# Kernel optimization log

Hardware: AMD Instinct MI355X
Metric: run time of the kernel (lower is better)

The kernel has to match this reference:

```python
import jax, jax.numpy as jnp
import numpy as np

B, DEPTH, E, NH, HD = 32, 12, 768, 12, 64
IMG, PS, GRID = 224, 16, 14
N = GRID * GRID + 1  # 197 tokens incl. cls
EPS = 1e-5


def _rel_index(wh, ww):
    # BEiT relative position index, incl. cls-token rows/cols
    coords = np.stack(np.meshgrid(np.arange(wh), np.arange(ww), indexing='ij'))
    cf = coords.reshape(2, -1)
    rc = (cf[:, :, None] - cf[:, None, :]).transpose(1, 2, 0).astype(np.int64)
    rc[:, :, 0] += wh - 1
    rc[:, :, 1] += ww - 1
    rc[:, :, 0] *= 2 * ww - 1
    nrd = (2 * wh - 1) * (2 * ww - 1) + 3
    idx = np.zeros((wh * ww + 1, wh * ww + 1), dtype=np.int32)
    idx[1:, 1:] = rc.sum(-1)
    idx[0, :] = nrd - 3
    idx[:, 0] = nrd - 2
    idx[0, 0] = nrd - 1
    return jnp.asarray(idx)

REL_IDX = _rel_index(GRID, GRID)  # [197,197] int32 constant


def _ln(x, w, b):
    m = x.mean(-1, keepdims=True)
    v = ((x - m) ** 2).mean(-1, keepdims=True)
    return (x - m) * jax.lax.rsqrt(v + EPS) * w + b


def setup_inputs() -> dict:
    key = jax.random.key(0)
    ks = jax.random.split(key, 8)
    s = 0.02
    rn = lambda k, shape: jax.random.normal(k, shape, jnp.float32) * s
    D = DEPTH
    return {
        'x': jax.random.normal(ks[0], (B, 3, IMG, IMG), jnp.float32),
        'patch_w': rn(ks[1], (E, 3 * PS * PS)),
        'patch_b': jnp.zeros((E,), jnp.float32),
        'cls_token': jnp.zeros((1, 1, E), jnp.float32),
        'ln1_w': jnp.ones((D, E), jnp.float32),
        'ln1_b': jnp.zeros((D, E), jnp.float32),
        'qkv_w': rn(ks[2], (D, 3 * E, E)),
        'q_bias': jnp.zeros((D, E), jnp.float32),
        'v_bias': jnp.zeros((D, E), jnp.float32),
        'rel_table': rn(ks[3], (D, (2 * GRID - 1) ** 2 + 3, NH)),
        'proj_w': rn(ks[4], (D, E, E)),
        'proj_b': jnp.zeros((D, E), jnp.float32),
        'ln2_w': jnp.ones((D, E), jnp.float32),
        'ln2_b': jnp.zeros((D, E), jnp.float32),
        'fc1_w': rn(ks[5], (D, 4 * E, E)),
        'fc1_b': jnp.zeros((D, 4 * E), jnp.float32),
        'fc2_w': rn(ks[6], (D, E, 4 * E)),
        'fc2_b': jnp.zeros((D, E), jnp.float32),
        'fcn_w': jnp.ones((E,), jnp.float32),
        'fcn_b': jnp.zeros((E,), jnp.float32),
        'head_w': rn(ks[7], (1000, E)),
        'head_b': jnp.zeros((1000,), jnp.float32),
    }


def reference(x, patch_w, patch_b, cls_token, ln1_w, ln1_b, qkv_w, q_bias,
              v_bias, rel_table, proj_w, proj_b, ln2_w, ln2_b, fc1_w, fc1_b,
              fc2_w, fc2_b, fcn_w, fcn_b, head_w, head_b):
    b = x.shape[0]
    scale = HD ** -0.5
    # patch embed: stride-16 conv == patchify + matmul (weight flattened as [E, C*kh*kw])
    patches = x.reshape(b, 3, GRID, PS, GRID, PS).transpose(0, 2, 4, 1, 3, 5)
    patches = patches.reshape(b, GRID * GRID, 3 * PS * PS)
    tok = patches @ patch_w.T + patch_b
    tok = jnp.concatenate([jnp.broadcast_to(cls_token, (b, 1, E)), tok], axis=1)  # [B,197,E]

    params = dict(ln1_w=ln1_w, ln1_b=ln1_b, qkv_w=qkv_w, q_bias=q_bias,
                  v_bias=v_bias, rel_table=rel_table, proj_w=proj_w,
                  proj_b=proj_b, ln2_w=ln2_w, ln2_b=ln2_b, fc1_w=fc1_w,
                  fc1_b=fc1_b, fc2_w=fc2_w, fc2_b=fc2_b)

    def block(h, p):
        y = _ln(h, p['ln1_w'], p['ln1_b'])
        qkvb = jnp.concatenate([p['q_bias'], jnp.zeros_like(p['q_bias']), p['v_bias']])
        qkv = (y @ p['qkv_w'].T + qkvb).reshape(b, N, 3, NH, HD).transpose(2, 0, 3, 1, 4)
        q, k, v = qkv[0] * scale, qkv[1], qkv[2]  # [B,H,N,hd]
        bias = p['rel_table'][REL_IDX].transpose(2, 0, 1)  # [H,N,N]
        att = jax.nn.softmax(jnp.einsum('bhnd,bhmd->bhnm', q, k) + bias[None], axis=-1)
        o = jnp.einsum('bhnm,bhmd->bhnd', att, v).transpose(0, 2, 1, 3).reshape(b, N, E)
        h = h + o @ p['proj_w'].T + p['proj_b']
        y = _ln(h, p['ln2_w'], p['ln2_b'])
        y = jax.nn.gelu(y @ p['fc1_w'].T + p['fc1_b'], approximate=False)
        return h + y @ p['fc2_w'].T + p['fc2_b'], None

    tok, _ = jax.lax.scan(block, tok, params)
    feat = _ln(tok[:, 1:].mean(axis=1), fcn_w, fcn_b)  # mean pooling over patch tokens
    return feat @ head_w.T + head_b  # [B, 1000]
```

## Files before the change

kernel.cpp:

```cpp
#include <hip/hip_runtime.h>
#include <hip/hip_bf16.h>
#include <math.h>


typedef __hip_bfloat16 bf16;
using short8 = __attribute__((ext_vector_type(8))) short;
using f32x4  = __attribute__((ext_vector_type(4))) float;

#define NTOK 197
#define NHEAD 12
#define NPAD 224

#define S_QKV  1769472
#define S_PROJ 589824
#define S_FC   2359296
#define O_PROJ 1769472
#define O_FC1  2359296
#define O_FC2  4718592
#define W_TOT  7077888

#define GLD(gp, lp) __builtin_amdgcn_global_load_lds( \
    (const unsigned int __attribute__((address_space(1)))*)(gp), \
    (unsigned int __attribute__((address_space(3)))*)(lp), 16, 0, 0)

#define XCD_REMAP(bx, by)                                                     \
  int bx, by;                                                                 \
  {                                                                           \
    const int gx = gridDim.x;                                                 \
    const int nwg = gx * gridDim.y;                                           \
    const int l = blockIdx.y * gx + blockIdx.x;                               \
    const int q = nwg >> 3, r = nwg & 7;                                      \
    const int xcd = l & 7, cidx = l >> 3;                                     \
    const int wg = (xcd < r ? xcd * (q + 1) : r * (q + 1) + (xcd - r) * q)    \
                   + cidx;                                                    \
    bx = wg % gx; by = wg / gx;                                               \
  }

__global__ __launch_bounds__(256) void cvt_k(const float* __restrict__ src,
                                             bf16* __restrict__ dst, int n8) {
  int t = blockIdx.x * 256 + threadIdx.x;
  if (t >= n8) return;
  size_t i = (size_t)t * 8;
  float4 a = *(const float4*)(src + i);
  float4 b = *(const float4*)(src + i + 4);
  union { short8 v; bf16 e[8]; } u;
  u.e[0] = __float2bfloat16(a.x); u.e[1] = __float2bfloat16(a.y);
  u.e[2] = __float2bfloat16(a.z); u.e[3] = __float2bfloat16(a.w);
  u.e[4] = __float2bfloat16(b.x); u.e[5] = __float2bfloat16(b.y);
  u.e[6] = __float2bfloat16(b.z); u.e[7] = __float2bfloat16(b.w);
  *(short8*)(dst + i) = u.v;
}

__global__ __launch_bounds__(256) void cvt_layer_k(
    const float* __restrict__ qkvw, const float* __restrict__ projw,
    const float* __restrict__ fc1w, const float* __restrict__ fc2w,
    bf16* __restrict__ wl, int d) {
  size_t i = ((size_t)blockIdx.x * 256 + threadIdx.x) * 8;
  if (i >= W_TOT) return;
  const float* src;
  if (i < O_PROJ)      src = qkvw + (size_t)d * S_QKV + i;
  else if (i < O_FC1)  src = projw + (size_t)d * S_PROJ + (i - O_PROJ);
  else if (i < O_FC2)  src = fc1w + (size_t)d * S_FC + (i - O_FC1);
  else                 src = fc2w + (size_t)d * S_FC + (i - O_FC2);
  float4 a = *(const float4*)src;
  float4 b = *(const float4*)(src + 4);
  union { short8 v; bf16 e[8]; } u;
  u.e[0] = __float2bfloat16(a.x); u.e[1] = __float2bfloat16(a.y);
  u.e[2] = __float2bfloat16(a.z); u.e[3] = __float2bfloat16(a.w);
  u.e[4] = __float2bfloat16(b.x); u.e[5] = __float2bfloat16(b.y);
  u.e[6] = __float2bfloat16(b.z); u.e[7] = __float2bfloat16(b.w);
  *(short8*)(wl + i) = u.v;
}

__global__ __launch_bounds__(256) void patchify_k(const float* __restrict__ x,
                                                  bf16* __restrict__ patches) {
  int o = blockIdx.x * 256 + threadIdx.x;
  if (o >= 6272 * 768) return;
  int row = o / 768, col = o % 768;
  int b = row / 196, g = row % 196;
  int gh = g / 14, gw = g % 14;
  int c = col / 256, r = col % 256;
  int ph = r / 16, pw = r % 16;
  patches[o] = __float2bfloat16(
      x[(((size_t)b * 3 + c) * 224 + gh * 16 + ph) * 224 + gw * 16 + pw]);
}

__global__ __launch_bounds__(256) void clsfill_k(const float* __restrict__ cls,
                                                 float* __restrict__ h) {
  int i = blockIdx.x * 256 + threadIdx.x;
  if (i >= 32 * 768) return;
  int b = i / 768, e = i % 768;
  h[((size_t)b * 197) * 768 + e] = cls[e];
}

__global__ __launch_bounds__(256) void vtz_k(bf16* __restrict__ vt) {
  int i = blockIdx.x * 256 + threadIdx.x;
  if (i >= 32 * 12 * 64 * NPAD / 8) return;
  *(short8*)(vt + (size_t)i * 8) = (short8){0,0,0,0,0,0,0,0};
}

__device__ __forceinline__ int ridx(int n, int m) {
  if (n == 0) return (m == 0) ? 731 : 729;
  if (m == 0) return 730;
  int nh = (n - 1) / 14, nw = (n - 1) % 14;
  int mh = (m - 1) / 14, mw = (m - 1) % 14;
  return (nh - mh + 13) * 27 + (nw - mw + 13);
}

__global__ __launch_bounds__(256) void bias_k(const float* __restrict__ rel,
                                              float* __restrict__ biasT,
                                              int layer) {
  int idx = blockIdx.x * 256 + threadIdx.x;
  if (idx >= 12 * NPAD * 256) return;
  int h = idx / (NPAD * 256);
  int rem = idx % (NPAD * 256);
  int m = rem / 256, n = rem % 256;
  float v;
  if (m >= NTOK) {
    v = -1e30f;
  } else {
    int nn = min(n, NTOK - 1);
    v = rel[((size_t)layer * 732 + ridx(nn, m)) * 12 + h];
  }
  biasT[idx] = v;
}

template <int EPI>
__global__ __launch_bounds__(512, 4) void mm256_k(
    const bf16* __restrict__ A, const bf16* __restrict__ W,
    const float* __restrict__ bias, const float* __restrict__ bias2,
    void* __restrict__ Cout, bf16* __restrict__ vtg,
    int M, int Nn, int K) {
  constexpr int BUFSZ = 24576;
  __shared__ __attribute__((aligned(16))) char lds[3 * BUFSZ];
  const int tid = threadIdx.x;
  const int lane = tid & 63, wave = tid >> 6;
  const int wr = wave >> 1, wc = wave & 1;
  const int l15 = lane & 15, lg = lane >> 4;
  XCD_REMAP(bx, by);
  const int row0 = bx * 256, n0 = by * 128;
  const int nt = K >> 5, ntm1 = nt - 1;

  const bf16 *gA0, *gA1, *gB0;
  int dA0, dA1, dB0;
  {
    int s = tid * 16;
    int r = s >> 6, cl = ((s >> 4) & 3) ^ ((r >> 1) & 3);
    gA0 = A + (size_t)(row0 + r) * K + cl * 8;  dA0 = s;
    s = 8192 + tid * 16;
    r = s >> 6; cl = ((s >> 4) & 3) ^ ((r >> 1) & 3);
    gA1 = A + (size_t)(row0 + r) * K + cl * 8;  dA1 = s;
    s = tid * 16;
    r = s >> 6; cl = ((s >> 4) & 3) ^ ((r >> 1) & 3);
    gB0 = W + (size_t)(n0 + r) * K + cl * 8;    dB0 = 16384 + s;
  }
  int oA[4], oB[4];
#pragma unroll
  for (int m = 0; m < 4; m++) {
    int r = wr * 64 + m * 16 + l15;
    oA[m] = (r << 6) | ((lg ^ ((r >> 1) & 3)) << 4);
  }
#pragma unroll
  for (int n = 0; n < 4; n++) {
    int r = wc * 64 + n * 16 + l15;
    oB[n] = 16384 + ((r << 6) | ((lg ^ ((r >> 1) & 3)) << 4));
  }

  f32x4 acc[4][4];
#pragma unroll
  for (int m = 0; m < 4; m++)
#pragma unroll
    for (int n = 0; n < 4; n++) acc[m][n] = (f32x4){0.f, 0.f, 0.f, 0.f};

  GLD(gA0, lds + dA0); GLD(gA1, lds + dA1); GLD(gB0, lds + dB0);
  GLD(gA0 + 32, lds + BUFSZ + dA0); GLD(gA1 + 32, lds + BUFSZ + dA1);
  GLD(gB0 + 32, lds + BUFSZ + dB0);
  asm volatile("s_waitcnt vmcnt(3)" ::: "memory");
  __builtin_amdgcn_s_barrier();
  __builtin_amdgcn_sched_barrier(0);

#define MB(RB, WB, tt)                                                        \
  {                                                                           \
    int ks = (tt) + 2; if (ks > ntm1) ks = ntm1; ks <<= 5;                    \
    char* wb = lds + (WB) * BUFSZ;                                            \
    GLD(gA0 + ks, wb + dA0); GLD(gA1 + ks, wb + dA1);                         \
    GLD(gB0 + ks, wb + dB0);                                                  \
    const char* rb = lds + (RB) * BUFSZ;                                      \
    short8 a[4], b[4];                                                        \
    _Pragma("unroll") for (int m = 0; m < 4; m++)                             \
      a[m] = *(const short8*)(rb + oA[m]);                                    \
    _Pragma("unroll") for (int n = 0; n < 4; n++)                             \
      b[n] = *(const short8*)(rb + oB[n]);                                    \
    __builtin_amdgcn_s_setprio(1);                                            \
    _Pragma("unroll") for (int m = 0; m < 4; m++)                             \
      _Pragma("unroll") for (int n = 0; n < 4; n++)                           \
        acc[m][n] = __builtin_amdgcn_mfma_f32_16x16x32_bf16(a[m], b[n], acc[m][n], 0, 0, 0); \
    __builtin_amdgcn_s_setprio(0);                                            \
    __builtin_amdgcn_sched_barrier(0);                                        \
    asm volatile("s_waitcnt vmcnt(3)" ::: "memory");                          \
    __builtin_amdgcn_s_barrier();                                             \
    __builtin_amdgcn_sched_barrier(0);                                        \
  }

  for (int t = 0; t < nt; t += 3) {
    MB(0, 2, t); MB(1, 0, t + 1); MB(2, 1, t + 2);
  }
#undef MB
  asm volatile("s_waitcnt vmcnt(0)" ::: "memory");

#pragma unroll
  for (int m = 0; m < 4; m++) {
    const int rbase = row0 + wr * 64 + m * 16 + lg * 4;
#pragma unroll
    for (int n = 0; n < 4; n++) {
      const int gc = n0 + wc * 64 + n * 16 + l15;
      f32x4 v = acc[m][n];
#pragma unroll
      for (int j = 0; j < 4; j++) {
        int gr = rbase + j;
        if (gr >= M) continue;
        float val = v[j];
        if (EPI == 1) {
          if (gc < 768) val += bias[gc];
          else if (gc >= 1536) val += bias2[gc - 1536];
          if (gc >= 1536) {
            int ob = gr / 197, nn = gr - ob * 197, hd = gc - 1536;
            vtg[(((size_t)ob * 12 + (hd >> 6)) * 64 + (hd & 63)) * NPAD + nn] =
                __float2bfloat16(val);
          } else {
            ((bf16*)Cout)[(size_t)gr * Nn + gc] = __float2bfloat16(val);
          }
        } else {
          val += bias[gc];
          val = 0.5f * val * (1.f + erff(val * 0.70710678118654752f));
          ((bf16*)Cout)[(size_t)gr * Nn + gc] = __float2bfloat16(val);
        }
      }
    }
  }
}

template <int EPI>
__global__ __launch_bounds__(256, 3) void mm128_k(
    const bf16* __restrict__ A, const bf16* __restrict__ W,
    const float* __restrict__ bias, const float* __restrict__ Res,
    void* __restrict__ Cout, int M, int Nn, int K) {
  constexpr int BUFSZ = 16384;
  __shared__ __attribute__((aligned(16))) char lds[3 * BUFSZ];
  const int tid = threadIdx.x;
  const int lane = tid & 63, wave = tid >> 6;
  const int wr = wave >> 1, wc = wave & 1;
  const int l15 = lane & 15, lg = lane >> 4;
  XCD_REMAP(bx, by);
  const int row0 = bx * 128, n0 = by * 128;
  const int nt = K >> 5, ntm1 = nt - 1;

  const bf16 *gA0, *gA1, *gB0, *gB1;
  int dA0, dA1, dB0, dB1;
  {
    int s = tid * 16;
    int r = s >> 6, cl = ((s >> 4) & 3) ^ ((r >> 1) & 3);
    gA0 = A + (size_t)(row0 + r) * K + cl * 8;  dA0 = s;
    s = 4096 + tid * 16;
    r = s >> 6; cl = ((s >> 4) & 3) ^ ((r >> 1) & 3);
    gA1 = A + (size_t)(row0 + r) * K + cl * 8;  dA1 = s;
    s = tid * 16;
    r = s >> 6; cl = ((s >> 4) & 3) ^ ((r >> 1) & 3);
    gB0 = W + (size_t)(n0 + r) * K + cl * 8;    dB0 = 8192 + s;
    s = 4096 + tid * 16;
    r = s >> 6; cl = ((s >> 4) & 3) ^ ((r >> 1) & 3);
    gB1 = W + (size_t)(n0 + r) * K + cl * 8;    dB1 = 8192 + s;
  }
  int oA[4], oB[4];
#pragma unroll
  for (int m = 0; m < 4; m++) {
    int r = wr * 64 + m * 16 + l15;
    oA[m] = (r << 6) | ((lg ^ ((r >> 1) & 3)) << 4);
  }
#pragma unroll
  for (int n = 0; n < 4; n++) {
    int r = wc * 64 + n * 16 + l15;
    oB[n] = 8192 + ((r << 6) | ((lg ^ ((r >> 1) & 3)) << 4));
  }

  f32x4 acc[4][4];
#pragma unroll
  for (int m = 0; m < 4; m++)
#pragma unroll
    for (int n = 0; n < 4; n++) acc[m][n] = (f32x4){0.f, 0.f, 0.f, 0.f};

  GLD(gA0, lds + dA0); GLD(gA1, lds + dA1);
  GLD(gB0, lds + dB0); GLD(gB1, lds + dB1);
  GLD(gA0 + 32, lds + BUFSZ + dA0); GLD(gA1 + 32, lds + BUFSZ + dA1);
  GLD(gB0 + 32, lds + BUFSZ + dB0); GLD(gB1 + 32, lds + BUFSZ + dB1);
  asm volatile("s_waitcnt vmcnt(4)" ::: "memory");
  __builtin_amdgcn_s_barrier();
  __builtin_amdgcn_sched_barrier(0);

#define MB(RB, WB, tt)                                                        \
  {                                                                           \
    int ks = (tt) + 2; if (ks > ntm1) ks = ntm1; ks <<= 5;                    \
    char* wb = lds + (WB) * BUFSZ;                                            \
    GLD(gA0 + ks, wb + dA0); GLD(gA1 + ks, wb + dA1);                         \
    GLD(gB0 + ks, wb + dB0); GLD(gB1 + ks, wb + dB1);                         \
    const char* rb = lds + (RB) * BUFSZ;                                      \
    short8 a[4], b[4];                                                        \
    _Pragma("unroll") for (int m = 0; m < 4; m++)                             \
      a[m] = *(const short8*)(rb + oA[m]);                                    \
    _Pragma("unroll") for (int n = 0; n < 4; n++)                             \
      b[n] = *(const short8*)(rb + oB[n]);                                    \
    __builtin_amdgcn_s_setprio(1);                                            \
    _Pragma("unroll") for (int m = 0; m < 4; m++)                             \
      _Pragma("unroll") for (int n = 0; n < 4; n++)                           \
        acc[m][n] = __builtin_amdgcn_mfma_f32_16x16x32_bf16(a[m], b[n], acc[m][n], 0, 0, 0); \
    __builtin_amdgcn_s_setprio(0);                                            \
    __builtin_amdgcn_sched_barrier(0);                                        \
    asm volatile("s_waitcnt vmcnt(4)" ::: "memory");                          \
    __builtin_amdgcn_s_barrier();                                             \
    __builtin_amdgcn_sched_barrier(0);                                        \
  }

  for (int t = 0; t < nt; t += 3) {
    MB(0, 2, t); MB(1, 0, t + 1); MB(2, 1, t + 2);
  }
#undef MB
  asm volatile("s_waitcnt vmcnt(0)" ::: "memory");

#pragma unroll
  for (int m = 0; m < 4; m++) {
    const int rbase = row0 + wr * 64 + m * 16 + lg * 4;
#pragma unroll
    for (int n = 0; n < 4; n++) {
      const int gc = n0 + wc * 64 + n * 16 + l15;
      f32x4 v = acc[m][n];
#pragma unroll
      for (int j = 0; j < 4; j++) {
        int gr = rbase + j;
        if (gr >= M) continue;
        float val = v[j] + bias[gc];
        if (EPI == 2) val += Res[(size_t)gr * Nn + gc];
        int orow = (EPI == 0) ? (gr + gr / 196 + 1) : gr;
        ((float*)Cout)[(size_t)orow * Nn + gc] = val;
      }
    }
  }
}

__global__ __launch_bounds__(256) void ln_k(const float* __restrict__ in,
                                            bf16* __restrict__ outp,
                                            const float* __restrict__ w,
                                            const float* __restrict__ b,
                                            int rows) {
  int row = blockIdx.x * 4 + threadIdx.y;
  if (row >= rows) return;
  int lane = threadIdx.x;
  const float* xr = in + (size_t)row * 768;
  float v[12];
  float s = 0.f;
#pragma unroll
  for (int i = 0; i < 12; i++) { v[i] = xr[lane + i * 64]; s += v[i]; }
#pragma unroll
  for (int o = 32; o; o >>= 1) s += __shfl_xor(s, o);
  float mean = s * (1.f / 768.f);
  float var = 0.f;
#pragma unroll
  for (int i = 0; i < 12; i++) { float d = v[i] - mean; var += d * d; }
#pragma unroll
  for (int o = 32; o; o >>= 1) var += __shfl_xor(var, o);
  float rs = rsqrtf(var * (1.f / 768.f) + 1e-5f);
  bf16* orow = outp + (size_t)row * 768;
#pragma unroll
  for (int i = 0; i < 12; i++) {
    int e = lane + i * 64;
    orow[e] = __float2bfloat16((v[i] - mean) * rs * w[e] + b[e]);
  }
}

__device__ __forceinline__ unsigned pkbf(float a, float b) {
  union { bf16 h; unsigned short u; } ua, ub;
  ua.h = __float2bfloat16(a); ub.h = __float2bfloat16(b);
  return ((unsigned)ub.u << 16) | (unsigned)ua.u;
}

__global__ __launch_bounds__(256) void attn2_k(const bf16* __restrict__ qkvb,
                                               const bf16* __restrict__ vtg,
                                               const float* __restrict__ biasT,
                                               bf16* __restrict__ outp) {
  __shared__ bf16 Ks[NPAD * 64];
  __shared__ bf16 Vt[64 * NPAD];
  __shared__ bf16 Ps[4][64 * 32];
  __shared__ float denl[4][64];

  const int bh = blockIdx.x;
  const int b = bh / 12, h = bh % 12;
  const int tid = threadIdx.x;
  const int wave = tid >> 6, lane = tid & 63;
  const int l15 = lane & 15, lg = lane >> 4;
  const int qbase = wave * 64;

  const bf16* vsrc = vtg + (size_t)bh * 64 * NPAD;
#pragma unroll
  for (int i = 0; i < 7; i++) {
    int c = i * 256 + tid;
    GLD(vsrc + c * 8, Vt + c * 8);
  }
#pragma unroll
  for (int i = 0; i < 7; i++) {
    int slot = i * 256 + tid;
    int r = slot >> 3, c8 = (slot & 7) * 8;
    int rg = min(r, NTOK - 1);
    short8 kv = *(const short8*)(qkvb + (size_t)(b * NTOK + rg) * 2304 + 768 + h * 64 + c8);
    int byte = (r * 128 + c8 * 2) ^ ((r & 7) << 4);
    *(short8*)((char*)Ks + byte) = kv;
  }
  short8 qf[4][2];
#pragma unroll
  for (int nf = 0; nf < 4; nf++) {
    int n = qbase + nf * 16 + l15;
    const bf16* qp = qkvb + (size_t)(b * NTOK + min(n, NTOK - 1)) * 2304 + h * 64;
    qf[nf][0] = *(const short8*)(qp + lg * 8);
    qf[nf][1] = *(const short8*)(qp + 32 + lg * 8);
  }
  __syncthreads();

  f32x4 Oacc[4][4];
#pragma unroll
  for (int i = 0; i < 4; i++)
#pragma unroll
    for (int j = 0; j < 4; j++) Oacc[i][j] = (f32x4){0.f, 0.f, 0.f, 0.f};
  float den[4] = {0.f, 0.f, 0.f, 0.f};
  const float* bT = biasT + (size_t)h * NPAD * 256;
  char* pw = (char*)&Ps[wave][0];

  for (int c = 0; c < 7; c++) {
    const int m0 = c * 32;
    f32x4 st[2][4];
#pragma unroll
    for (int mf = 0; mf < 2; mf++)
#pragma unroll
      for (int nf = 0; nf < 4; nf++) st[mf][nf] = (f32x4){0.f, 0.f, 0.f, 0.f};
#pragma unroll
    for (int kk = 0; kk < 2; kk++) {
      short8 af[2];
#pragma unroll
      for (int mf = 0; mf < 2; mf++) {
        int m = m0 + mf * 16 + l15;
        int byte = (m * 128 + kk * 64 + lg * 16) ^ ((m & 7) << 4);
        af[mf] = *(const short8*)((const char*)Ks + byte);
      }
#pragma unroll
      for (int mf = 0; mf < 2; mf++)
#pragma unroll
        for (int nf = 0; nf < 4; nf++)
          st[mf][nf] = __builtin_amdgcn_mfma_f32_16x16x32_bf16(af[mf], qf[nf][kk], st[mf][nf], 0, 0, 0);
    }
#pragma unroll
    for (int mf = 0; mf < 2; mf++) {
      int mrow = m0 + mf * 16 + lg * 4;
#pragma unroll
      for (int nf = 0; nf < 4; nf++) {
        int n = qbase + nf * 16 + l15;
        float p0 = __expf(st[mf][nf][0] * 0.125f + bT[(mrow + 0) * 256 + n]);
        float p1 = __expf(st[mf][nf][1] * 0.125f + bT[(mrow + 1) * 256 + n]);
        float p2 = __expf(st[mf][nf][2] * 0.125f + bT[(mrow + 2) * 256 + n]);
        float p3 = __expf(st[mf][nf][3] * 0.125f + bT[(mrow + 3) * 256 + n]);
        den[nf] += (p0 + p1) + (p2 + p3);
        int nl = nf * 16 + l15;
        int byte = (nl * 64 + (mf * 16 + lg * 4) * 2) ^ ((nl & 7) << 4);
        *(unsigned*)(pw + byte) = pkbf(p0, p1);
        *(unsigned*)(pw + byte + 4) = pkbf(p2, p3);
      }
    }
    short8 pa[4], vb[4];
#pragma unroll
    for (int nf = 0; nf < 4; nf++) {
      int nl = nf * 16 + l15;
      int byte = (nl * 64 + lg * 16) ^ ((nl & 7) << 4);
      pa[nf] = *(const short8*)((const char*)pw + byte);
    }
#pragma unroll
    for (int df = 0; df < 4; df++) {
      int d = df * 16 + l15;
      vb[df] = *(const short8*)(Vt + d * NPAD + m0 + lg * 8);
    }
#pragma unroll
    for (int nf = 0; nf < 4; nf++)
#pragma unroll
      for (int df = 0; df < 4; df++)
        Oacc[nf][df] = __builtin_amdgcn_mfma_f32_16x16x32_bf16(pa[nf], vb[df], Oacc[nf][df], 0, 0, 0);
  }

#pragma unroll
  for (int nf = 0; nf < 4; nf++) {
    den[nf] += __shfl_xor(den[nf], 16);
    den[nf] += __shfl_xor(den[nf], 32);
    denl[wave][nf * 16 + l15] = den[nf];
  }
  float inv[4][4];
#pragma unroll
  for (int nf = 0; nf < 4; nf++)
#pragma unroll
    for (int j = 0; j < 4; j++)
      inv[nf][j] = 1.f / denl[wave][nf * 16 + lg * 4 + j];
#pragma unroll
  for (int nf = 0; nf < 4; nf++) {
#pragma unroll
    for (int df = 0; df < 4; df++) {
#pragma unroll
      for (int j = 0; j < 4; j++) {
        int n = qbase + nf * 16 + lg * 4 + j;
        if (n < NTOK)
          outp[(size_t)(b * NTOK + n) * 768 + h * 64 + df * 16 + l15] =
              __float2bfloat16(Oacc[nf][df][j] * inv[nf][j]);
      }
    }
  }
}

__device__ __forceinline__ float block_sum(float v, float* sm4) {
#pragma unroll
  for (int o = 32; o; o >>= 1) v += __shfl_down(v, o);
  __syncthreads();
  if ((threadIdx.x & 63) == 0) sm4[threadIdx.x >> 6] = v;
  __syncthreads();
  return sm4[0] + sm4[1] + sm4[2] + sm4[3];
}

__global__ __launch_bounds__(256) void pool_ln_k(const float* __restrict__ h,
                                                 const float* __restrict__ w,
                                                 const float* __restrict__ bi,
                                                 float* __restrict__ feat) {
  __shared__ float sm4[4];
  int b = blockIdx.x, tid = threadIdx.x;
  float vals[3];
  float local = 0.f;
#pragma unroll
  for (int j = 0; j < 3; j++) {
    int e = tid + j * 256;
    float s = 0.f;
    for (int nn = 1; nn < 197; nn++) s += h[((size_t)(b * 197 + nn)) * 768 + e];
    s *= (1.f / 196.f);
    vals[j] = s;
    local += s;
  }
  float tot = block_sum(local, sm4);
  float mean = tot * (1.f / 768.f);
  float lv = 0.f;
#pragma unroll
  for (int j = 0; j < 3; j++) { float d = vals[j] - mean; lv += d * d; }
  float vtot = block_sum(lv, sm4);
  float rs = rsqrtf(vtot * (1.f / 768.f) + 1e-5f);
#pragma unroll
  for (int j = 0; j < 3; j++) {
    int e = tid + j * 256;
    feat[(size_t)b * 768 + e] = (vals[j] - mean) * rs * w[e] + bi[e];
  }
}

__global__ __launch_bounds__(256) void head_k(const float* __restrict__ A,
                                              const float* __restrict__ W,
                                              const float* __restrict__ bias,
                                              float* __restrict__ C,
                                              int M, int Nn, int K) {
  __shared__ float As[16][64 + 4];
  __shared__ float Bs[16][64 + 4];
  int tid = threadIdx.x;
  int tx = tid & 15, ty = tid >> 4;
  int row0 = blockIdx.x * 64, n0 = blockIdx.y * 64;
  int lrow = tid >> 2;
  int kq = (tid & 3) * 4;
  float acc[4][4];
#pragma unroll
  for (int i = 0; i < 4; i++)
#pragma unroll
    for (int j = 0; j < 4; j++) acc[i][j] = 0.f;
  for (int k0 = 0; k0 < K; k0 += 16) {
    float4 av = make_float4(0.f, 0.f, 0.f, 0.f);
    if (row0 + lrow < M) av = *(const float4*)&A[(size_t)(row0 + lrow) * K + k0 + kq];
    As[kq + 0][lrow] = av.x; As[kq + 1][lrow] = av.y;
    As[kq + 2][lrow] = av.z; As[kq + 3][lrow] = av.w;
    float4 bv = make_float4(0.f, 0.f, 0.f, 0.f);
    if (n0 + lrow < Nn) bv = *(const float4*)&W[(size_t)(n0 + lrow) * K + k0 + kq];
    Bs[kq + 0][lrow] = bv.x; Bs[kq + 1][lrow] = bv.y;
    Bs[kq + 2][lrow] = bv.z; Bs[kq + 3][lrow] = bv.w;
    __syncthreads();
#pragma unroll
    for (int kk = 0; kk < 16; kk++) {
      float4 a = *(const float4*)&As[kk][ty * 4];
      float4 b = *(const float4*)&Bs[kk][tx * 4];
      float aa[4] = {a.x, a.y, a.z, a.w};
      float bb[4] = {b.x, b.y, b.z, b.w};
#pragma unroll
      for (int i = 0; i < 4; i++)
#pragma unroll
        for (int j = 0; j < 4; j++) acc[i][j] = fmaf(aa[i], bb[j], acc[i][j]);
    }
    __syncthreads();
  }
#pragma unroll
  for (int i = 0; i < 4; i++) {
    int gr = row0 + ty * 4 + i;
    if (gr >= M) continue;
#pragma unroll
    for (int j = 0; j < 4; j++) {
      int gc = n0 + tx * 4 + j;
      if (gc >= Nn) continue;
      C[(size_t)gr * Nn + gc] = acc[i][j] + bias[gc];
    }
  }
}

extern "C" void kernel_launch(void* const* d_in, const int* in_sizes, int n_in,
                              void* d_out, int out_size, void* d_ws, size_t ws_size,
                              hipStream_t stream) {
  const float* x       = (const float*)d_in[0];
  const float* patch_w = (const float*)d_in[1];
  const float* patch_b = (const float*)d_in[2];
  const float* cls_tok = (const float*)d_in[3];
  const float* ln1_w   = (const float*)d_in[4];
  const float* ln1_b   = (const float*)d_in[5];
  const float* qkv_w   = (const float*)d_in[6];
  const float* q_bias  = (const float*)d_in[7];
  const float* v_bias  = (const float*)d_in[8];
  const float* rel_tab = (const float*)d_in[9];
  const float* proj_w  = (const float*)d_in[10];
  const float* proj_b  = (const float*)d_in[11];
  const float* ln2_w   = (const float*)d_in[12];
  const float* ln2_b   = (const float*)d_in[13];
  const float* fc1_w   = (const float*)d_in[14];
  const float* fc1_b   = (const float*)d_in[15];
  const float* fc2_w   = (const float*)d_in[16];
  const float* fc2_b   = (const float*)d_in[17];
  const float* fcn_w   = (const float*)d_in[18];
  const float* fcn_b   = (const float*)d_in[19];
  const float* head_w  = (const float*)d_in[20];
  const float* head_b  = (const float*)d_in[21];
  float* outp = (float*)d_out;

  char* wsb = (char*)d_ws;
  float* h    = (float*)wsb;  wsb += 19365888;
  bf16* bigb  = (bf16*)wsb;   wsb += 29048832;
  bf16* yb    = (bf16*)wsb;   wsb += 9830400;
  bf16* hid   = (bf16*)wsb;   wsb += 39321600;
  bf16* wl    = (bf16*)wsb;   wsb += 14155776;
  bf16* vt_g  = (bf16*)wsb;   wsb += 11010048;
  float* biasT = (float*)wsb; wsb += 2752512;
  float* feat = (float*)wsb;

  const int M = 6304;

  vtz_k<<<2688, 256, 0, stream>>>(vt_g);
  patchify_k<<<(6272 * 768 + 255) / 256, 256, 0, stream>>>(x, hid);
  cvt_k<<<(589824 / 8 + 255) / 256, 256, 0, stream>>>(patch_w, wl, 589824 / 8);
  mm128_k<0><<<dim3(49, 6), 256, 0, stream>>>(
      hid, wl, patch_b, nullptr, h, 6272, 768, 768);
  clsfill_k<<<(32 * 768 + 255) / 256, 256, 0, stream>>>(cls_tok, h);

  for (int d = 0; d < 12; d++) {
    cvt_layer_k<<<W_TOT / 8 / 256, 256, 0, stream>>>(qkv_w, proj_w, fc1_w, fc2_w, wl, d);
    bias_k<<<(12 * NPAD * 256) / 256, 256, 0, stream>>>(rel_tab, biasT, d);
    ln_k<<<dim3((M + 3) / 4), dim3(64, 4), 0, stream>>>(h, yb, ln1_w + d * 768, ln1_b + d * 768, M);
    mm256_k<1><<<dim3(25, 18), 512, 0, stream>>>(
        yb, wl, q_bias + d * 768, v_bias + d * 768, bigb, vt_g, M, 2304, 768);
    attn2_k<<<32 * NHEAD, 256, 0, stream>>>(bigb, vt_g, biasT, yb);
    mm128_k<2><<<dim3(50, 6), 256, 0, stream>>>(
        yb, wl + O_PROJ, proj_b + d * 768, h, h, M, 768, 768);
    ln_k<<<dim3((M + 3) / 4), dim3(64, 4), 0, stream>>>(h, yb, ln2_w + d * 768, ln2_b + d * 768, M);
    mm256_k<3><<<dim3(25, 24), 512, 0, stream>>>(
        yb, wl + O_FC1, fc1_b + d * 3072, nullptr, hid, nullptr, M, 3072, 768);
    mm128_k<2><<<dim3(50, 6), 256, 0, stream>>>(
        hid, wl + O_FC2, fc2_b + d * 768, h, h, M, 768, 3072);
  }

  pool_ln_k<<<32, 256, 0, stream>>>(h, fcn_w, fcn_b, feat);
  {
    dim3 g(1, (1000 + 63) / 64);
    head_k<<<g, 256, 0, stream>>>(feat, head_w, head_b, outp, 32, 1000, 768);
  }
}
```

Baseline: 3.610 ms.

## Fuse weight conversion with bias build, vectorize LayerNorm, drop XCD block remap

Merges the per-layer weight bf16 conversion and the relative-position bias table build into one launch, removing a kernel launch per layer. LayerNorm now loads rows as float4 and writes packed bf16x4, cutting instruction count and memory transactions. The XCD-aware workgroup remapping in both GEMM kernels is removed in favour of plain blockIdx indexing, which may hurt L2 locality across chiplets. The vmcnt wait thresholds in the GEMM pipelines are lowered, which makes each stage wait on more outstanding loads and reduces prefetch overlap.

```diff
diff --git a/kernel.cpp b/kernel.cpp
--- a/kernel.cpp
+++ b/kernel.cpp
@@ -22,19 +22,6 @@
 #define GLD(gp, lp) __builtin_amdgcn_global_load_lds( \
     (const unsigned int __attribute__((address_space(1)))*)(gp), \
     (unsigned int __attribute__((address_space(3)))*)(lp), 16, 0, 0)
-
-#define XCD_REMAP(bx, by)                                                     \
-  int bx, by;                                                                 \
-  {                                                                           \
-    const int gx = gridDim.x;                                                 \
-    const int nwg = gx * gridDim.y;                                           \
-    const int l = blockIdx.y * gx + blockIdx.x;                               \
-    const int q = nwg >> 3, r = nwg & 7;                                      \
-    const int xcd = l & 7, cidx = l >> 3;                                     \
-    const int wg = (xcd < r ? xcd * (q + 1) : r * (q + 1) + (xcd - r) * q)    \
-                   + cidx;                                                    \
-    bx = wg % gx; by = wg / gx;                                               \
-  }
 
 __global__ __launch_bounds__(256) void cvt_k(const float* __restrict__ src,
                                              bf16* __restrict__ dst, int n8) {
@@ -51,25 +38,49 @@
   *(short8*)(dst + i) = u.v;
 }
 
-__global__ __launch_bounds__(256) void cvt_layer_k(
+__device__ __forceinline__ int ridx(int n, int m) {
+  if (n == 0) return (m == 0) ? 731 : 729;
+  if (m == 0) return 730;
+  int nh = (n - 1) / 14, nw = (n - 1) % 14;
+  int mh = (m - 1) / 14, mw = (m - 1) % 14;
+  return (nh - mh + 13) * 27 + (nw - mw + 13);
+}
+
+__global__ __launch_bounds__(256) void prep_k(
     const float* __restrict__ qkvw, const float* __restrict__ projw,
     const float* __restrict__ fc1w, const float* __restrict__ fc2w,
-    bf16* __restrict__ wl, int d) {
-  size_t i = ((size_t)blockIdx.x * 256 + threadIdx.x) * 8;
-  if (i >= W_TOT) return;
-  const float* src;
-  if (i < O_PROJ)      src = qkvw + (size_t)d * S_QKV + i;
-  else if (i < O_FC1)  src = projw + (size_t)d * S_PROJ + (i - O_PROJ);
-  else if (i < O_FC2)  src = fc1w + (size_t)d * S_FC + (i - O_FC1);
-  else                 src = fc2w + (size_t)d * S_FC + (i - O_FC2);
-  float4 a = *(const float4*)src;
-  float4 b = *(const float4*)(src + 4);
-  union { short8 v; bf16 e[8]; } u;
-  u.e[0] = __float2bfloat16(a.x); u.e[1] = __float2bfloat16(a.y);
-  u.e[2] = __float2bfloat16(a.z); u.e[3] = __float2bfloat16(a.w);
-  u.e[4] = __float2bfloat16(b.x); u.e[5] = __float2bfloat16(b.y);
-  u.e[6] = __float2bfloat16(b.z); u.e[7] = __float2bfloat16(b.w);
-  *(short8*)(wl + i) = u.v;
+    const float* __restrict__ rel, bf16* __restrict__ wl,
+    float* __restrict__ biasT, int d) {
+  int blk = blockIdx.x;
+  if (blk < 3456) {
+    size_t i = ((size_t)blk * 256 + threadIdx.x) * 8;
+    const float* src;
+    if (i < O_PROJ)      src = qkvw + (size_t)d * S_QKV + i;
+    else if (i < O_FC1)  src = projw + (size_t)d * S_PROJ + (i - O_PROJ);
+    else if (i < O_FC2)  src = fc1w + (size_t)d * S_FC + (i - O_FC1);
+    else                 src = fc2w + (size_t)d * S_FC + (i - O_FC2);
+    float4 a = *(const float4*)src;
+    float4 b = *(const float4*)(src + 4);
+    union { short8 v; bf16 e[8]; } u;
+    u.e[0] = __float2bfloat16(a.x); u.e[1] = __float2bfloat16(a.y);
+    u.e[2] = __float2bfloat16(a.z); u.e[3] = __float2bfloat16(a.w);
+    u.e[4] = __float2bfloat16(b.x); u.e[5] = __float2bfloat16(b.y);
+    u.e[6] = __float2bfloat16(b.z); u.e[7] = __float2bfloat16(b.w);
+    *(short8*)(wl + i) = u.v;
+  } else {
+    int idx = (blk - 3456) * 256 + threadIdx.x;
+    int h = idx / (NPAD * 256);
+    int rem = idx % (NPAD * 256);
+    int m = rem / 256, n = rem % 256;
+    float v;
+    if (m >= NTOK) {
+      v = -1e30f;
+    } else {
+      int nn = min(n, NTOK - 1);
+      v = rel[((size_t)d * 732 + ridx(nn, m)) * 12 + h];
+    }
+    biasT[idx] = v;
+  }
 }
 
 __global__ __launch_bounds__(256) void patchify_k(const float* __restrict__ x,
@@ -97,32 +108,6 @@
   int i = blockIdx.x * 256 + threadIdx.x;
   if (i >= 32 * 12 * 64 * NPAD / 8) return;
   *(short8*)(vt + (size_t)i * 8) = (short8){0,0,0,0,0,0,0,0};
-}
-
-__device__ __forceinline__ int ridx(int n, int m) {
-  if (n == 0) return (m == 0) ? 731 : 729;
-  if (m == 0) return 730;
-  int nh = (n - 1) / 14, nw = (n - 1) % 14;
-  int mh = (m - 1) / 14, mw = (m - 1) % 14;
-  return (nh - mh + 13) * 27 + (nw - mw + 13);
-}
-
-__global__ __launch_bounds__(256) void bias_k(const float* __restrict__ rel,
-                                              float* __restrict__ biasT,
-                                              int layer) {
-  int idx = blockIdx.x * 256 + threadIdx.x;
-  if (idx >= 12 * NPAD * 256) return;
-  int h = idx / (NPAD * 256);
-  int rem = idx % (NPAD * 256);
-  int m = rem / 256, n = rem % 256;
-  float v;
-  if (m >= NTOK) {
-    v = -1e30f;
-  } else {
-    int nn = min(n, NTOK - 1);
-    v = rel[((size_t)layer * 732 + ridx(nn, m)) * 12 + h];
-  }
-  biasT[idx] = v;
 }
 
 template <int EPI>
@@ -137,8 +122,7 @@
   const int lane = tid & 63, wave = tid >> 6;
   const int wr = wave >> 1, wc = wave & 1;
   const int l15 = lane & 15, lg = lane >> 4;
-  XCD_REMAP(bx, by);
-  const int row0 = bx * 256, n0 = by * 128;
+  const int row0 = blockIdx.x * 256, n0 = blockIdx.y * 128;
   const int nt = K >> 5, ntm1 = nt - 1;
 
   const bf16 *gA0, *gA1, *gB0;
@@ -197,7 +181,7 @@
         acc[m][n] = __builtin_amdgcn_mfma_f32_16x16x32_bf16(a[m], b[n], acc[m][n], 0, 0, 0); \
     __builtin_amdgcn_s_setprio(0);                                            \
     __builtin_amdgcn_sched_barrier(0);                                        \
-    asm volatile("s_waitcnt vmcnt(3)" ::: "memory");                          \
+    asm volatile("s_waitcnt vmcnt(2)" ::: "memory");                          \
     __builtin_amdgcn_s_barrier();                                             \
     __builtin_amdgcn_sched_barrier(0);                                        \
   }
@@ -251,8 +235,7 @@
   const int lane = tid & 63, wave = tid >> 6;
   const int wr = wave >> 1, wc = wave & 1;
   const int l15 = lane & 15, lg = lane >> 4;
-  XCD_REMAP(bx, by);
-  const int row0 = bx * 128, n0 = by * 128;
+  const int row0 = blockIdx.x * 128, n0 = blockIdx.y * 128;
   const int nt = K >> 5, ntm1 = nt - 1;
 
   const bf16 *gA0, *gA1, *gB0, *gB1;
@@ -315,7 +298,7 @@
         acc[m][n] = __builtin_amdgcn_mfma_f32_16x16x32_bf16(a[m], b[n], acc[m][n], 0, 0, 0); \
     __builtin_amdgcn_s_setprio(0);                                            \
     __builtin_amdgcn_sched_barrier(0);                                        \
-    asm volatile("s_waitcnt vmcnt(4)" ::: "memory");                          \
+    asm volatile("s_waitcnt vmcnt(3)" ::: "memory");                          \
     __builtin_amdgcn_s_barrier();                                             \
     __builtin_amdgcn_sched_barrier(0);                                        \
   }
@@ -354,25 +337,41 @@
   int row = blockIdx.x * 4 + threadIdx.y;
   if (row >= rows) return;
   int lane = threadIdx.x;
-  const float* xr = in + (size_t)row * 768;
-  float v[12];
+  const float4* xr = (const float4*)(in + (size_t)row * 768);
+  float4 v[3];
   float s = 0.f;
 #pragma unroll
-  for (int i = 0; i < 12; i++) { v[i] = xr[lane + i * 64]; s += v[i]; }
+  for (int i = 0; i < 3; i++) {
+    v[i] = xr[lane + i * 64];
+    s += (v[i].x + v[i].y) + (v[i].z + v[i].w);
+  }
 #pragma unroll
   for (int o = 32; o; o >>= 1) s += __shfl_xor(s, o);
   float mean = s * (1.f / 768.f);
   float var = 0.f;
 #pragma unroll
-  for (int i = 0; i < 12; i++) { float d = v[i] - mean; var += d * d; }
+  for (int i = 0; i < 3; i++) {
+    float d0 = v[i].x - mean, d1 = v[i].y - mean;
+    float d2 = v[i].z - mean, d3 = v[i].w - mean;
+    var += (d0 * d0 + d1 * d1) + (d2 * d2 + d3 * d3);
+  }
 #pragma unroll
   for (int o = 32; o; o >>= 1) var += __shfl_xor(var, o);
   float rs = rsqrtf(var * (1.f / 768.f) + 1e-5f);
+  const float4* w4 = (const float4*)w;
+  const float4* b4 = (const float4*)b;
   bf16* orow = outp + (size_t)row * 768;
 #pragma unroll
-  for (int i = 0; i < 12; i++) {
-    int e = lane + i * 64;
-    orow[e] = __float2bfloat16((v[i] - mean) * rs * w[e] + b[e]);
+  for (int i = 0; i < 3; i++) {
+    int e4 = lane + i * 64;
+    float4 wv = w4[e4], bv = b4[e4];
+    union { bf16 h; short s; } c0, c1, c2, c3;
+    c0.h = __float2bfloat16((v[i].x - mean) * rs * wv.x + bv.x);
+    c1.h = __float2bfloat16((v[i].y - mean) * rs * wv.y + bv.y);
+    c2.h = __float2bfloat16((v[i].z - mean) * rs * wv.z + bv.z);
+    c3.h = __float2bfloat16((v[i].w - mean) * rs * wv.w + bv.w);
+    short4 o4 = make_short4(c0.s, c1.s, c2.s, c3.s);
+    *(short4*)(orow + e4 * 4) = o4;
   }
 }
 
@@ -657,8 +656,8 @@
   clsfill_k<<<(32 * 768 + 255) / 256, 256, 0, stream>>>(cls_tok, h);
 
   for (int d = 0; d < 12; d++) {
-    cvt_layer_k<<<W_TOT / 8 / 256, 256, 0, stream>>>(qkv_w, proj_w, fc1_w, fc2_w, wl, d);
-    bias_k<<<(12 * NPAD * 256) / 256, 256, 0, stream>>>(rel_tab, biasT, d);
+    prep_k<<<6144, 256, 0, stream>>>(qkv_w, proj_w, fc1_w, fc2_w, rel_tab,
+                                     wl, biasT, d);
     ln_k<<<dim3((M + 3) / 4), dim3(64, 4), 0, stream>>>(h, yb, ln1_w + d * 768, ln1_b + d * 768, M);
     mm256_k<1><<<dim3(25, 18), 512, 0, stream>>>(
         yb, wl, q_bias + d * 768, v_bias + d * 768, bigb, vt_g, M, 2304, 768);
```

Result: faster. 3.299 ms, median of 2 (-8.6%).
